# Performance work log

Hardware: AMD Instinct MI355X
Metric: run time of the kernel (lower is better)

The kernel has to match this reference:

```python
import jax, jax.numpy as jnp
import numpy as np

E = 8           # num experts
T = 8192        # total tokens
K = 4096        # input dim
N = 4096        # output dim


def setup_inputs() -> dict:
    key = jax.random.key(0)
    k1, k2, k3 = jax.random.split(key, 3)
    a = jax.random.normal(k1, (T, K), dtype=jnp.float32)
    b = jax.random.normal(k2, (E, N, K), dtype=jnp.float32) * 0.02  # column-major expert weights
    c = jnp.zeros((T, N), dtype=jnp.float32)
    inner = jnp.sort(jax.random.randint(k3, (E - 1,), 0, T))
    seg_indptr = jnp.concatenate([jnp.zeros((1,), jnp.int64),
                                  inner.astype(jnp.int64),
                                  jnp.full((1,), T, jnp.int64)])
    weight_indices = jnp.arange(E, dtype=jnp.int64)
    return {"a": a, "b": b, "c": c, "seg_indptr": seg_indptr,
            "weight_indices": weight_indices, "batch_size": E}


def reference(a, b, c, seg_indptr, weight_indices, batch_size):
    # Grouped GEMM: tokens in segment [seg_indptr[e], seg_indptr[e+1]) use
    # expert weight b[weight_indices[e]] (column-major: out = a @ W.T).
    t = a.shape[0]
    b_sel = b[weight_indices]                                  # [E, N, K]
    out_all = jnp.einsum('tk,enk->etn', a, b_sel)              # [E, T, N]
    tok = jnp.arange(t)
    # expert id of each token from sorted segment boundaries
    eid = jnp.clip(jnp.searchsorted(seg_indptr, tok, side='right') - 1,
                   0, batch_size - 1)
    return out_all[eid, tok]                                   # [T, N]
```

## Files before the change

### kernel.cpp

```cpp
#include <hip/hip_runtime.h>
#include <hip/hip_bf16.h>

typedef float f32x4 __attribute__((ext_vector_type(4)));
typedef short bf16x8 __attribute__((ext_vector_type(8)));
typedef unsigned short u16;

constexpr int T_TOK = 8192;
constexpr int KDIM  = 4096;
constexpr int NDIM  = 4096;
constexpr int NE    = 8;

constexpr long long TA = (long long)T_TOK * KDIM;
constexpr long long TB = (long long)NE * NDIM * KDIM;

__device__ __forceinline__ u16 f2bf(float f) {
  unsigned u = __builtin_bit_cast(unsigned, f);
  u += 0x7FFFu + ((u >> 16) & 1u);
  return (u16)(u >> 16);
}

__global__ __launch_bounds__(256)
void cvt_bf16(const float* __restrict__ A, const float* __restrict__ B,
              u16* __restrict__ oA, u16* __restrict__ oB) {
  const long long nv = (TA + TB) >> 3;
  const long long stride = (long long)gridDim.x * blockDim.x;
  for (long long i = (long long)blockIdx.x * blockDim.x + threadIdx.x; i < nv; i += stride) {
    const long long e = i << 3;
    const float* s;
    u16* d;
    if (e < TA) { s = A + e;        d = oA + e; }
    else        { s = B + (e - TA); d = oB + (e - TA); }
    f32x4 v0 = ((const f32x4*)s)[0];
    f32x4 v1 = ((const f32x4*)s)[1];
    bf16x8 p;
    #pragma unroll
    for (int j = 0; j < 4; ++j) p[j]     = (short)f2bf(v0[j]);
    #pragma unroll
    for (int j = 0; j < 4; ++j) p[4 + j] = (short)f2bf(v1[j]);
    *(bf16x8*)d = p;
  }
}

__device__ __forceinline__ void gload16(const u16* g, const u16* l) {
  __builtin_amdgcn_global_load_lds(
      (const __attribute__((address_space(1))) void*)g,
      (__attribute__((address_space(3))) void*)l, 16, 0, 0);
}

constexpr int BM2 = 256, BN2 = 256, BK2 = 64;
constexpr int NKT2 = KDIM / BK2;
constexpr int NTN2 = NDIM / BN2;
constexpr int MT2  = T_TOK / BM2 + NE;
constexpr int NWG_TOT = MT2 * NTN2;
constexpr int NWG_L1  = 512;
constexpr int NWG_ALL = NWG_L1 + (NWG_TOT - NWG_L1) * 2;
constexpr int ASZ  = BM2 * BK2;
constexpr int HSZ  = ASZ / 2;

__device__ __forceinline__ bool decode_tile(const int* segp, int mt,
                                            int& e, int& segs, int& sege, int& mloc) {
  e = -1;
  int acc0 = 0, sp = segp[0];
  #pragma unroll
  for (int i = 0; i < NE; ++i) {
    int sn = segp[i + 1];
    int nti = (sn - sp + BM2 - 1) / BM2;
    if (e < 0 && mt < acc0 + nti) { e = i; mloc = mt - acc0; segs = sp; sege = sn; }
    acc0 += nti; sp = sn;
  }
  return e >= 0;
}

__global__ __launch_bounds__(512, 2)
void gg_merged(const u16* __restrict__ Abf, const u16* __restrict__ Bbf,
               float* __restrict__ C, const int* __restrict__ segp,
               const int* __restrict__ widx)
{
  extern __shared__ u16 sm[];

  const int tid = threadIdx.x, lane = tid & 63, wid = tid >> 6;
  const int bid0 = (int)blockIdx.x;

  if (bid0 < NWG_L1) {
    u16* sA = sm;
    u16* sB = sm + 2 * ASZ;

    int bid = (bid0 & 7) * (NWG_L1 / 8) + (bid0 >> 3);
    const int nt = bid % NTN2;
    const int mt = bid / NTN2;

    int e, segs, sege, mloc;
    if (!decode_tile(segp, mt, e, segs, sege, mloc)) return;

    const int row_base = segs + mloc * BM2;
    const int col_base = nt * BN2;
    const u16* __restrict__ W = Bbf + (long long)widx[e] * ((long long)NDIM * KDIM);

    const int wr = wid >> 2, wc = wid & 3;

    const int sg = (((lane & 7) ^ (lane >> 3)) << 3);
    const int rr = wid * 8 + (lane >> 3);
    int oA[2][2], oB[2][2];
    #pragma unroll
    for (int h = 0; h < 2; ++h)
      #pragma unroll
      for (int i = 0; i < 2; ++i) {
        oA[h][i] = min(row_base + h * 128 + i * 64 + rr, T_TOK - 1) * KDIM + sg;
        oB[h][i] = (col_base + h * 128 + i * 64 + rr) * KDIM + sg;
      }

    const int g0  = (lane >> 4) ^ (lane & 7);
    const int g1  = g0 ^ 4;
    const int rA0 = (wr * 64 + (lane & 15)) * BK2 + g0 * 8;
    const int rA1 = (wr * 64 + (lane & 15)) * BK2 + g1 * 8;
    const int rB0 = (wc * 32 + (lane & 15)) * BK2 + g0 * 8;
    const int rB1 = (wc * 32 + (lane & 15)) * BK2 + g1 * 8;

    f32x4 acc[8][4];
    #pragma unroll
    for (int m = 0; m < 8; ++m)
      #pragma unroll
      for (int n = 0; n < 4; ++n)
        acc[m][n] = (f32x4){0.f, 0.f, 0.f, 0.f};

    bf16x8 aF[4][2], bF0[2][2], bF1[2][2];

    auto STGA = [&](int bbuf, int h, int t) __attribute__((always_inline)) {
      gload16(Abf + oA[h][0] + t * BK2, sA + bbuf * ASZ + h * HSZ + wid * 512);
      gload16(Abf + oA[h][1] + t * BK2, sA + bbuf * ASZ + h * HSZ + 4096 + wid * 512);
    };
    auto STGB = [&](int bbuf, int h, int t) __attribute__((always_inline)) {
      gload16(W + oB[h][0] + t * BK2, sB + bbuf * ASZ + h * HSZ + wid * 512);
      gload16(W + oB[h][1] + t * BK2, sB + bbuf * ASZ + h * HSZ + 4096 + wid * 512);
    };
    auto LDA = [&](int bbuf, int mh) __attribute__((always_inline)) {
      #pragma unroll
      for (int j = 0; j < 4; ++j) {
        const u16* p = sA + bbuf * ASZ + mh * HSZ + j * 16 * BK2;
        aF[j][0] = *(const bf16x8*)(p + rA0);
        aF[j][1] = *(const bf16x8*)(p + rA1);
      }
    };
    auto LDB = [&](int bbuf, int nh, bf16x8 (&bF)[2][2]) __attribute__((always_inline)) {
      #pragma unroll
      for (int i = 0; i < 2; ++i) {
        const u16* p = sB + bbuf * ASZ + nh * HSZ + i * 16 * BK2;
        bF[i][0] = *(const bf16x8*)(p + rB0);
        bF[i][1] = *(const bf16x8*)(p + rB1);
      }
    };
    auto MF = [&](int mh, int nh, bf16x8 (&bF)[2][2]) __attribute__((always_inline)) {
      __builtin_amdgcn_s_setprio(1);
      #pragma unroll
      for (int j = 0; j < 4; ++j)
        #pragma unroll
        for (int i = 0; i < 2; ++i) {
          acc[mh * 4 + j][nh * 2 + i] = __builtin_amdgcn_mfma_f32_16x16x32_bf16(
              aF[j][0], bF[i][0], acc[mh * 4 + j][nh * 2 + i], 0, 0, 0);
          acc[mh * 4 + j][nh * 2 + i] = __builtin_amdgcn_mfma_f32_16x16x32_bf16(
              aF[j][1], bF[i][1], acc[mh * 4 + j][nh * 2 + i], 0, 0, 0);
        }
      __builtin_amdgcn_s_setprio(0);
    };

    STGA(0, 0, 0); STGB(0, 0, 0); STGA(0, 1, 0); STGB(0, 1, 0);
    STGA(1, 0, 1); STGB(1, 0, 1);
    asm volatile("s_waitcnt vmcnt(4)" ::: "memory");
    __builtin_amdgcn_s_barrier();

    for (int t = 0; t < NKT2; ++t) {
      const int bb = t & 1, nb = bb ^ 1;

      LDA(bb, 0); LDB(bb, 0, bF0); LDB(bb, 1, bF1);
      if (t + 1 < NKT2) { STGA(nb, 1, t + 1); STGB(nb, 1, t + 1); }
      MF(0, 0, bF0); MF(0, 1, bF1);
      __builtin_amdgcn_s_barrier();

      LDA(bb, 1);
      if (t + 2 < NKT2) { STGA(bb, 0, t + 2); STGB(bb, 0, t + 2); }
      MF(1, 0, bF0); MF(1, 1, bF1);
      if (t + 2 < NKT2) {
        asm volatile("s_waitcnt vmcnt(4)" ::: "memory");
      } else {
        asm volatile("s_waitcnt vmcnt(0)" ::: "memory");
      }
      __builtin_amdgcn_s_barrier();
    }

    #pragma unroll
    for (int m = 0; m < 8; ++m) {
      const int r0 = row_base + (m >> 2) * 128 + wr * 64 + (m & 3) * 16 + ((lane >> 4) << 2);
      #pragma unroll
      for (int j = 0; j < 4; ++j) {
        const int r = r0 + j;
        if (r < sege) {
          float* cp = C + (long long)r * NDIM + col_base + (lane & 15);
          #pragma unroll
          for (int n = 0; n < 4; ++n)
            cp[(n >> 1) * 128 + wc * 32 + (n & 1) * 16] = acc[m][n][j];
        }
      }
    }
  } else {
    u16* sA = sm;
    u16* sB = sm + 2 * HSZ;

    const int b = bid0 - NWG_L1;
    const int swz = (b & 7) * 32 + (b >> 3);
    const int tile = NWG_L1 + (swz >> 1);
    const int mh   = swz & 1;
    const int nt = tile % NTN2;
    const int mt = tile / NTN2;

    int e, segs, sege, mloc;
    if (!decode_tile(segp, mt, e, segs, sege, mloc)) return;

    const int row_base = segs + mloc * BM2 + mh * 128;
    const int col_base = nt * BN2;
    const u16* __restrict__ W = Bbf + (long long)widx[e] * ((long long)NDIM * KDIM);

    const int wr = wid >> 2, wc = wid & 3;

    const int sg = (((lane & 7) ^ (lane >> 3)) << 3);
    const int rr = wid * 8 + (lane >> 3);
    int oA[2], oB[4];
    #pragma unroll
    for (int i = 0; i < 2; ++i)
      oA[i] = min(row_base + i * 64 + rr, T_TOK - 1) * KDIM + sg;
    #pragma unroll
    for (int i = 0; i < 4; ++i)
      oB[i] = (col_base + i * 64 + rr) * KDIM + sg;

    const int g0  = (lane >> 4) ^ (lane & 7);
    const int g1  = g0 ^ 4;
    const int rA0 = (wr * 64 + (lane & 15)) * BK2 + g0 * 8;
    const int rA1 = (wr * 64 + (lane & 15)) * BK2 + g1 * 8;
    const int rB0 = (wc * 64 + (lane & 15)) * BK2 + g0 * 8;
    const int rB1 = (wc * 64 + (lane & 15)) * BK2 + g1 * 8;

    f32x4 acc[4][4];
    #pragma unroll
    for (int m = 0; m < 4; ++m)
      #pragma unroll
      for (int n = 0; n < 4; ++n)
        acc[m][n] = (f32x4){0.f, 0.f, 0.f, 0.f};

    auto STAGE = [&](int bbuf, int t) __attribute__((always_inline)) {
      gload16(Abf + oA[0] + t * BK2, sA + bbuf * HSZ + wid * 512);
      gload16(Abf + oA[1] + t * BK2, sA + bbuf * HSZ + 4096 + wid * 512);
      #pragma unroll
      for (int i = 0; i < 4; ++i)
        gload16(W + oB[i] + t * BK2, sB + bbuf * ASZ + i * 4096 + wid * 512);
    };

    STAGE(0, 0); STAGE(1, 1);
    asm volatile("s_waitcnt vmcnt(6)" ::: "memory");
    __builtin_amdgcn_s_barrier();

    for (int t = 0; t < NKT2; ++t) {
      const int bb = t & 1;

      bf16x8 aF[4][2], bF[4][2];
      #pragma unroll
      for (int m = 0; m < 4; ++m) {
        const u16* p = sA + bb * HSZ + m * 16 * BK2;
        aF[m][0] = *(const bf16x8*)(p + rA0);
        aF[m][1] = *(const bf16x8*)(p + rA1);
      }
      #pragma unroll
      for (int n = 0; n < 4; ++n) {
        const u16* p = sB + bb * ASZ + n * 16 * BK2;
        bF[n][0] = *(const bf16x8*)(p + rB0);
        bF[n][1] = *(const bf16x8*)(p + rB1);
      }

      asm volatile("s_waitcnt lgkmcnt(0)" ::: "memory");
      __builtin_amdgcn_s_barrier();

      if (t + 2 < NKT2) STAGE(bb, t + 2);

      __builtin_amdgcn_s_setprio(1);
      #pragma unroll
      for (int m = 0; m < 4; ++m)
        #pragma unroll
        for (int n = 0; n < 4; ++n) {
          acc[m][n] = __builtin_amdgcn_mfma_f32_16x16x32_bf16(aF[m][0], bF[n][0], acc[m][n], 0, 0, 0);
          acc[m][n] = __builtin_amdgcn_mfma_f32_16x16x32_bf16(aF[m][1], bF[n][1], acc[m][n], 0, 0, 0);
        }
      __builtin_amdgcn_s_setprio(0);

      if (t + 2 < NKT2) {
        asm volatile("s_waitcnt vmcnt(6)" ::: "memory");
      } else {
        asm volatile("s_waitcnt vmcnt(0)" ::: "memory");
      }
      __builtin_amdgcn_s_barrier();
    }

    #pragma unroll
    for (int m = 0; m < 4; ++m) {
      const int r0 = row_base + wr * 64 + m * 16 + ((lane >> 4) << 2);
      #pragma unroll
      for (int j = 0; j < 4; ++j) {
        const int r = r0 + j;
        if (r < sege) {
          float* cp = C + (long long)r * NDIM + col_base + wc * 64 + (lane & 15);
          #pragma unroll
          for (int n = 0; n < 4; ++n)
            cp[n * 16] = acc[m][n][j];
        }
      }
    }
  }
}

constexpr int BM = 128, BN = 128, BK = 32;
constexpr int LDKF = BK + 8;
constexpr int NTN = NDIM / BN;
constexpr int MT_MAX = T_TOK / BM + NE;
constexpr int NKT = KDIM / BK;
constexpr int NWG = MT_MAX * NTN;

__global__ __launch_bounds__(256, 2)
void grouped_gemm_fused(const float* __restrict__ A, const float* __restrict__ B,
                        float* __restrict__ C, const int* __restrict__ segp,
                        const int* __restrict__ widx)
{
  __shared__ u16 lA[2][BM][LDKF];
  __shared__ u16 lB[2][BN][LDKF];

  const int nt = blockIdx.x % NTN;
  const int mt = blockIdx.x / NTN;

  int e = -1, segs = 0, sege = 0, mloc = 0;
  {
    int acc0 = 0, sp = segp[0];
    #pragma unroll
    for (int i = 0; i < NE; ++i) {
      int sn = segp[i + 1];
      int nti = (sn - sp + BM - 1) / BM;
      if (e < 0 && mt < acc0 + nti) { e = i; mloc = mt - acc0; segs = sp; sege = sn; }
      acc0 += nti; sp = sn;
    }
  }
  if (e < 0) return;

  const int row_base = segs + mloc * BM;
  const int col_base = nt * BN;
  const float* __restrict__ W = B + (long long)widx[e] * NDIM * KDIM;

  const int tid  = threadIdx.x;
  const int lane = tid & 63;
  const int wid  = tid >> 6;
  const int wr   = wid >> 1;
  const int wc   = wid & 1;

  const int srow = tid >> 1;
  const int scol = (tid & 1) << 4;
  const int arow = min(row_base + srow, T_TOK - 1);
  const float* __restrict__ aptr = A + (long long)arow * KDIM + scol;
  const float* __restrict__ bptr = W + (long long)(col_base + srow) * KDIM + scol;

  f32x4 sa[4], sb[4];
  f32x4 acc[4][4];
  #pragma unroll
  for (int m = 0; m < 4; ++m)
    #pragma unroll
    for (int n = 0; n < 4; ++n)
      acc[m][n] = (f32x4){0.f, 0.f, 0.f, 0.f};

  const int frow = lane & 15;
  const int fk   = (lane >> 4) << 3;

  auto load_tiles = [&](int kt) {
    const float* ap = aptr + kt * BK;
    const float* bp = bptr + kt * BK;
    #pragma unroll
    for (int i = 0; i < 4; ++i) sa[i] = *(const f32x4*)(ap + i * 4);
    #pragma unroll
    for (int i = 0; i < 4; ++i) sb[i] = *(const f32x4*)(bp + i * 4);
  };
  auto conv_write = [&](int buf) {
    u16* wa = &lA[buf][srow][scol];
    u16* wb = &lB[buf][srow][scol];
    bf16x8 p;
    #pragma unroll
    for (int j = 0; j < 8; ++j) p[j] = (short)f2bf(sa[j >> 2][j & 3]);
    *(bf16x8*)(wa) = p;
    #pragma unroll
    for (int j = 0; j < 8; ++j) p[j] = (short)f2bf(sa[2 + (j >> 2)][j & 3]);
    *(bf16x8*)(wa + 8) = p;
    #pragma unroll
    for (int j = 0; j < 8; ++j) p[j] = (short)f2bf(sb[j >> 2][j & 3]);
    *(bf16x8*)(wb) = p;
    #pragma unroll
    for (int j = 0; j < 8; ++j) p[j] = (short)f2bf(sb[2 + (j >> 2)][j & 3]);
    *(bf16x8*)(wb + 8) = p;
  };

  load_tiles(0);
  conv_write(0);
  __syncthreads();

  int cur = 0;
  for (int kt = 0; kt < NKT; ++kt) {
    const bool more = (kt + 1 < NKT);
    if (more) load_tiles(kt + 1);

    bf16x8 af[4], bfr[4];
    #pragma unroll
    for (int m = 0; m < 4; ++m)
      af[m] = *(const bf16x8*)&lA[cur][wr * 64 + m * 16 + frow][fk];
    #pragma unroll
    for (int n = 0; n < 4; ++n)
      bfr[n] = *(const bf16x8*)&lB[cur][wc * 64 + n * 16 + frow][fk];

    if (more) conv_write(cur ^ 1);

    #pragma unroll
    for (int m = 0; m < 4; ++m)
      #pragma unroll
      for (int n = 0; n < 4; ++n)
        acc[m][n] = __builtin_amdgcn_mfma_f32_16x16x32_bf16(af[m], bfr[n], acc[m][n], 0, 0, 0);

    __syncthreads();
    cur ^= 1;
  }

  const int crow0 = row_base + wr * 64;
  const int ccol  = col_base + wc * 64 + (lane & 15);
  const int rsub  = (lane >> 4) << 2;
  #pragma unroll
  for (int m = 0; m < 4; ++m) {
    #pragma unroll
    for (int j = 0; j < 4; ++j) {
      const int r = crow0 + m * 16 + rsub + j;
      if (r < sege) {
        #pragma unroll
        for (int n = 0; n < 4; ++n)
          C[(long long)r * NDIM + ccol + n * 16] = acc[m][n][j];
      }
    }
  }
}

extern "C" void kernel_launch(void* const* d_in, const int* in_sizes, int n_in,
                              void* d_out, int out_size, void* d_ws, size_t ws_size,
                              hipStream_t stream) {
  const float* A   = (const float*)d_in[0];
  const float* B   = (const float*)d_in[1];
  const int* segp  = (const int*)d_in[3];
  const int* widx  = (const int*)d_in[4];
  float* C = (float*)d_out;

  const size_t need = (size_t)(TA + TB) * sizeof(u16);
  if (ws_size >= need) {
    u16* oA = (u16*)d_ws;
    u16* oB = oA + TA;
    cvt_bf16<<<dim3(2048), dim3(256), 0, stream>>>(A, B, oA, oB);
    (void)hipFuncSetAttribute((const void*)gg_merged,
                              hipFuncAttributeMaxDynamicSharedMemorySize,
                              2 * 2 * ASZ * (int)sizeof(u16));
    gg_merged<<<dim3(NWG_ALL), dim3(512), 2 * 2 * ASZ * sizeof(u16), stream>>>(
        oA, oB, C, segp, widx);
  } else {
    grouped_gemm_fused<<<dim3(NWG), dim3(256), 0, stream>>>(A, B, C, segp, widx);
  }
}
```

Before: 472.0 us.

## Fuse expert-weight fp32-to-bf16 conversion into the grouped GEMM mainloop

Stops pre-converting the full expert weight tensor to bf16 in a separate pass. The GEMM now loads fp32 weight tiles into registers, converts them to bf16 and writes them into swizzled LDS, pipelined one k-step ahead; only the activations are still pre-converted. This drops the write and re-read of a bf16 copy of B (and its conversion launch), at the cost of reading fp32 weights repeatedly across M tiles (twice the bytes per load), extra VGPRs for the staging registers and more VALU and LDS-store work inside the mainloop.

```diff
diff --git a/kernel.cpp b/kernel.cpp
--- a/kernel.cpp
+++ b/kernel.cpp
@@ -3,6 +3,7 @@
 
 typedef float f32x4 __attribute__((ext_vector_type(4)));
 typedef short bf16x8 __attribute__((ext_vector_type(8)));
+typedef short bf16x4 __attribute__((ext_vector_type(4)));
 typedef unsigned short u16;
 
 constexpr int T_TOK = 8192;
@@ -20,24 +21,19 @@
 }
 
 __global__ __launch_bounds__(256)
-void cvt_bf16(const float* __restrict__ A, const float* __restrict__ B,
-              u16* __restrict__ oA, u16* __restrict__ oB) {
-  const long long nv = (TA + TB) >> 3;
+void cvt_bf16_A(const float* __restrict__ A, u16* __restrict__ oA) {
+  const long long nv = TA >> 3;
   const long long stride = (long long)gridDim.x * blockDim.x;
   for (long long i = (long long)blockIdx.x * blockDim.x + threadIdx.x; i < nv; i += stride) {
     const long long e = i << 3;
-    const float* s;
-    u16* d;
-    if (e < TA) { s = A + e;        d = oA + e; }
-    else        { s = B + (e - TA); d = oB + (e - TA); }
-    f32x4 v0 = ((const f32x4*)s)[0];
-    f32x4 v1 = ((const f32x4*)s)[1];
+    f32x4 v0 = ((const f32x4*)(A + e))[0];
+    f32x4 v1 = ((const f32x4*)(A + e))[1];
     bf16x8 p;
     #pragma unroll
     for (int j = 0; j < 4; ++j) p[j]     = (short)f2bf(v0[j]);
     #pragma unroll
     for (int j = 0; j < 4; ++j) p[4 + j] = (short)f2bf(v1[j]);
-    *(bf16x8*)d = p;
+    *(bf16x8*)(oA + e) = p;
   }
 }
 
@@ -72,7 +68,7 @@
 }
 
 __global__ __launch_bounds__(512, 2)
-void gg_merged(const u16* __restrict__ Abf, const u16* __restrict__ Bbf,
+void gg_merged(const u16* __restrict__ Abf, const float* __restrict__ Bf,
                float* __restrict__ C, const int* __restrict__ segp,
                const int* __restrict__ widx)
 {
@@ -94,20 +90,40 @@
 
     const int row_base = segs + mloc * BM2;
     const int col_base = nt * BN2;
-    const u16* __restrict__ W = Bbf + (long long)widx[e] * ((long long)NDIM * KDIM);
+    const float* __restrict__ W = Bf + (long long)widx[e] * ((long long)NDIM * KDIM);
 
     const int wr = wid >> 2, wc = wid & 3;
 
     const int sg = (((lane & 7) ^ (lane >> 3)) << 3);
     const int rr = wid * 8 + (lane >> 3);
-    int oA[2][2], oB[2][2];
+    int oA[2][2];
     #pragma unroll
     for (int h = 0; h < 2; ++h)
       #pragma unroll
-      for (int i = 0; i < 2; ++i) {
+      for (int i = 0; i < 2; ++i)
         oA[h][i] = min(row_base + h * 128 + i * 64 + rr, T_TOK - 1) * KDIM + sg;
-        oB[h][i] = (col_base + h * 128 + i * 64 + rr) * KDIM + sg;
-      }
+
+    const int brow_l = (lane >> 4);
+    const int bchunk = lane & 15;
+    f32x4 breg[8];
+    auto BISSUE = [&](int t) __attribute__((always_inline)) {
+      #pragma unroll
+      for (int j = 0; j < 8; ++j) {
+        const int r = wid * 32 + j * 4 + brow_l;
+        breg[j] = *(const f32x4*)(W + (long long)(col_base + r) * KDIM + t * BK2 + bchunk * 4);
+      }
+    };
+    auto BCVT = [&](int bbuf) __attribute__((always_inline)) {
+      #pragma unroll
+      for (int j = 0; j < 8; ++j) {
+        const int r = wid * 32 + j * 4 + brow_l;
+        bf16x4 p;
+        #pragma unroll
+        for (int k = 0; k < 4; ++k) p[k] = (short)f2bf(breg[j][k]);
+        const int g = (bchunk >> 1) ^ (r & 7);
+        *(bf16x4*)(sB + bbuf * ASZ + r * 64 + g * 8 + (bchunk & 1) * 4) = p;
+      }
+    };
 
     const int g0  = (lane >> 4) ^ (lane & 7);
     const int g1  = g0 ^ 4;
@@ -128,10 +144,6 @@
     auto STGA = [&](int bbuf, int h, int t) __attribute__((always_inline)) {
       gload16(Abf + oA[h][0] + t * BK2, sA + bbuf * ASZ + h * HSZ + wid * 512);
       gload16(Abf + oA[h][1] + t * BK2, sA + bbuf * ASZ + h * HSZ + 4096 + wid * 512);
-    };
-    auto STGB = [&](int bbuf, int h, int t) __attribute__((always_inline)) {
-      gload16(W + oB[h][0] + t * BK2, sB + bbuf * ASZ + h * HSZ + wid * 512);
-      gload16(W + oB[h][1] + t * BK2, sB + bbuf * ASZ + h * HSZ + 4096 + wid * 512);
     };
     auto LDA = [&](int bbuf, int mh) __attribute__((always_inline)) {
       #pragma unroll
@@ -163,27 +175,32 @@
       __builtin_amdgcn_s_setprio(0);
     };
 
-    STGA(0, 0, 0); STGB(0, 0, 0); STGA(0, 1, 0); STGB(0, 1, 0);
-    STGA(1, 0, 1); STGB(1, 0, 1);
-    asm volatile("s_waitcnt vmcnt(4)" ::: "memory");
+    STGA(0, 0, 0); STGA(0, 1, 0);
+    BISSUE(0);
+    STGA(1, 0, 1);
+    asm volatile("s_waitcnt vmcnt(2)" ::: "memory");
+    BCVT(0);
+    asm volatile("s_waitcnt lgkmcnt(0)" ::: "memory");
     __builtin_amdgcn_s_barrier();
 
     for (int t = 0; t < NKT2; ++t) {
       const int bb = t & 1, nb = bb ^ 1;
 
       LDA(bb, 0); LDB(bb, 0, bF0); LDB(bb, 1, bF1);
-      if (t + 1 < NKT2) { STGA(nb, 1, t + 1); STGB(nb, 1, t + 1); }
+      if (t + 1 < NKT2) { STGA(nb, 1, t + 1); BISSUE(t + 1); }
       MF(0, 0, bF0); MF(0, 1, bF1);
       __builtin_amdgcn_s_barrier();
 
       LDA(bb, 1);
-      if (t + 2 < NKT2) { STGA(bb, 0, t + 2); STGB(bb, 0, t + 2); }
-      MF(1, 0, bF0); MF(1, 1, bF1);
+      if (t + 2 < NKT2) STGA(bb, 0, t + 2);
       if (t + 2 < NKT2) {
-        asm volatile("s_waitcnt vmcnt(4)" ::: "memory");
+        asm volatile("s_waitcnt vmcnt(2)" ::: "memory");
       } else {
         asm volatile("s_waitcnt vmcnt(0)" ::: "memory");
       }
+      if (t + 1 < NKT2) BCVT(nb);
+      MF(1, 0, bF0); MF(1, 1, bF1);
+      asm volatile("s_waitcnt lgkmcnt(0)" ::: "memory");
       __builtin_amdgcn_s_barrier();
     }
 
@@ -217,19 +234,38 @@
 
     const int row_base = segs + mloc * BM2 + mh * 128;
     const int col_base = nt * BN2;
-    const u16* __restrict__ W = Bbf + (long long)widx[e] * ((long long)NDIM * KDIM);
+    const float* __restrict__ W = Bf + (long long)widx[e] * ((long long)NDIM * KDIM);
 
     const int wr = wid >> 2, wc = wid & 3;
 
     const int sg = (((lane & 7) ^ (lane >> 3)) << 3);
     const int rr = wid * 8 + (lane >> 3);
-    int oA[2], oB[4];
+    int oA[2];
     #pragma unroll
     for (int i = 0; i < 2; ++i)
       oA[i] = min(row_base + i * 64 + rr, T_TOK - 1) * KDIM + sg;
-    #pragma unroll
-    for (int i = 0; i < 4; ++i)
-      oB[i] = (col_base + i * 64 + rr) * KDIM + sg;
+
+    const int brow_l = (lane >> 4);
+    const int bchunk = lane & 15;
+    f32x4 breg[8];
+    auto BISSUE = [&](int t) __attribute__((always_inline)) {
+      #pragma unroll
+      for (int j = 0; j < 8; ++j) {
+        const int r = wid * 32 + j * 4 + brow_l;
+        breg[j] = *(const f32x4*)(W + (long long)(col_base + r) * KDIM + t * BK2 + bchunk * 4);
+      }
+    };
+    auto BCVT = [&](int bbuf) __attribute__((always_inline)) {
+      #pragma unroll
+      for (int j = 0; j < 8; ++j) {
+        const int r = wid * 32 + j * 4 + brow_l;
+        bf16x4 p;
+        #pragma unroll
+        for (int k = 0; k < 4; ++k) p[k] = (short)f2bf(breg[j][k]);
+        const int g = (bchunk >> 1) ^ (r & 7);
+        *(bf16x4*)(sB + bbuf * ASZ + r * 64 + g * 8 + (bchunk & 1) * 4) = p;
+      }
+    };
 
     const int g0  = (lane >> 4) ^ (lane & 7);
     const int g1  = g0 ^ 4;
@@ -245,20 +281,21 @@
       for (int n = 0; n < 4; ++n)
         acc[m][n] = (f32x4){0.f, 0.f, 0.f, 0.f};
 
-    auto STAGE = [&](int bbuf, int t) __attribute__((always_inline)) {
+    auto STAGE_A = [&](int bbuf, int t) __attribute__((always_inline)) {
       gload16(Abf + oA[0] + t * BK2, sA + bbuf * HSZ + wid * 512);
       gload16(Abf + oA[1] + t * BK2, sA + bbuf * HSZ + 4096 + wid * 512);
-      #pragma unroll
-      for (int i = 0; i < 4; ++i)
-        gload16(W + oB[i] + t * BK2, sB + bbuf * ASZ + i * 4096 + wid * 512);
-    };
-
-    STAGE(0, 0); STAGE(1, 1);
-    asm volatile("s_waitcnt vmcnt(6)" ::: "memory");
+    };
+
+    STAGE_A(0, 0);
+    BISSUE(0);
+    STAGE_A(1, 1);
+    asm volatile("s_waitcnt vmcnt(2)" ::: "memory");
+    BCVT(0);
+    asm volatile("s_waitcnt lgkmcnt(0)" ::: "memory");
     __builtin_amdgcn_s_barrier();
 
     for (int t = 0; t < NKT2; ++t) {
-      const int bb = t & 1;
+      const int bb = t & 1, nb = bb ^ 1;
 
       bf16x8 aF[4][2], bF[4][2];
       #pragma unroll
@@ -273,11 +310,18 @@
         bF[n][0] = *(const bf16x8*)(p + rB0);
         bF[n][1] = *(const bf16x8*)(p + rB1);
       }
+      if (t + 1 < NKT2) BISSUE(t + 1);
 
       asm volatile("s_waitcnt lgkmcnt(0)" ::: "memory");
       __builtin_amdgcn_s_barrier();
 
-      if (t + 2 < NKT2) STAGE(bb, t + 2);
+      if (t + 2 < NKT2) STAGE_A(bb, t + 2);
+      if (t + 2 < NKT2) {
+        asm volatile("s_waitcnt vmcnt(2)" ::: "memory");
+      } else {
+        asm volatile("s_waitcnt vmcnt(0)" ::: "memory");
+      }
+      if (t + 1 < NKT2) BCVT(nb);
 
       __builtin_amdgcn_s_setprio(1);
       #pragma unroll
@@ -289,11 +333,7 @@
         }
       __builtin_amdgcn_s_setprio(0);
 
-      if (t + 2 < NKT2) {
-        asm volatile("s_waitcnt vmcnt(6)" ::: "memory");
-      } else {
-        asm volatile("s_waitcnt vmcnt(0)" ::: "memory");
-      }
+      asm volatile("s_waitcnt lgkmcnt(0)" ::: "memory");
       __builtin_amdgcn_s_barrier();
     }
 
@@ -453,16 +493,15 @@
   const int* widx  = (const int*)d_in[4];
   float* C = (float*)d_out;
 
-  const size_t need = (size_t)(TA + TB) * sizeof(u16);
+  const size_t need = (size_t)TA * sizeof(u16);
   if (ws_size >= need) {
     u16* oA = (u16*)d_ws;
-    u16* oB = oA + TA;
-    cvt_bf16<<<dim3(2048), dim3(256), 0, stream>>>(A, B, oA, oB);
+    cvt_bf16_A<<<dim3(1024), dim3(256), 0, stream>>>(A, oA);
     (void)hipFuncSetAttribute((const void*)gg_merged,
                               hipFuncAttributeMaxDynamicSharedMemorySize,
                               2 * 2 * ASZ * (int)sizeof(u16));
     gg_merged<<<dim3(NWG_ALL), dim3(512), 2 * 2 * ASZ * sizeof(u16), stream>>>(
-        oA, oB, C, segp, widx);
+        oA, B, C, segp, widx);
   } else {
     grouped_gemm_fused<<<dim3(NWG), dim3(256), 0, stream>>>(A, B, C, segp, widx);
   }
```

Result: slower. 862.3 us (+82.7%).
